# Performance work log

Hardware: AMD Instinct MI355X
Metric: run time of the kernel (lower is better)

Reference implementation:

```python
import jax, jax.numpy as jnp
import numpy as np

B, S, H = 2, 2048, 4096
NH, HD = 32, 128          # heads, head_dim = H // NH
ROPE_THETA = 10000.0
CLIP_QKV = 8.0
SCALE = HD ** -0.5


def setup_inputs() -> dict:
    key = jax.random.key(0)
    k1, k2, k3 = jax.random.split(key, 3)
    hidden_states = jax.random.normal(k1, (B, S, H), dtype=jnp.float32)
    positions = jnp.arange(S, dtype=jnp.int32)
    # 0.02 init scale keeps qkv magnitudes realistic so the +/-8 clamp rarely saturates
    w_qkv = jax.random.normal(k2, (3 * H, H), dtype=jnp.float32) * 0.02
    w_o = jax.random.normal(k3, (H, H), dtype=jnp.float32) * 0.02
    return {"hidden_states": hidden_states, "positions": positions,
            "w_qkv": w_qkv, "w_o": w_o}


def _rope(x, positions):
    # x: [B, S, NH, HD]; neox-style rotary over full head_dim
    half = HD // 2
    inv_freq = 1.0 / (ROPE_THETA ** (jnp.arange(0, half, dtype=jnp.float32) / half))
    ang = positions.astype(jnp.float32)[:, None] * inv_freq[None, :]  # [S, half]
    cos = jnp.cos(ang)[None, :, None, :]
    sin = jnp.sin(ang)[None, :, None, :]
    x1, x2 = x[..., :half], x[..., half:]
    return jnp.concatenate([x1 * cos - x2 * sin, x2 * cos + x1 * sin], axis=-1)


def reference(hidden_states, positions, w_qkv, w_o):
    # fused QKV projection (no bias) + clamp
    qkv = jnp.einsum('bsh,oh->bso', hidden_states, w_qkv)
    qkv = jnp.clip(qkv, -CLIP_QKV, CLIP_QKV)
    q, k, v = jnp.split(qkv, 3, axis=-1)            # each [B, S, H]
    q = q.reshape(B, S, NH, HD)
    k = k.reshape(B, S, NH, HD)
    v = v.reshape(B, S, NH, HD)
    q = _rope(q, positions)
    k = _rope(k, positions)
    # causal attention
    scores = jnp.einsum('bqhd,bkhd->bhqk', q, k) * SCALE
    causal = jnp.tril(jnp.ones((S, S), dtype=bool))
    scores = jnp.where(causal[None, None], scores, jnp.finfo(scores.dtype).min)
    probs = jax.nn.softmax(scores, axis=-1)
    attn = jnp.einsum('bhqk,bkhd->bqhd', probs, v).reshape(B, S, H)
    return jnp.einsum('bsh,oh->bso', attn, w_o)
```

## Files before the change

kernel.cpp:

```cpp
#include <hip/hip_runtime.h>
#include <hip/hip_bf16.h>

#define BATCH 2
#define SEQ 2048
#define HID 4096
#define NHEAD 32
#define HDIM 128
#define BH (BATCH*NHEAD)
#define MROWS (BATCH*SEQ)
#define ATT_SCALE 0.08838834764831845f

typedef __attribute__((ext_vector_type(8))) short bf16x8;
typedef __attribute__((ext_vector_type(4))) float f32x4;

__device__ __forceinline__ float bf2f(short x){
  union { float f; unsigned u; } v; v.u = ((unsigned)(unsigned short)x) << 16; return v.f;
}
__device__ __forceinline__ short f2bf(float f){
  union { float f; unsigned u; } v; v.f = f;
  unsigned r = v.u + 0x7fffu + ((v.u >> 16) & 1u);
  return (short)(r >> 16);
}
__device__ __forceinline__ void gload_lds16(const void* g, void* l){
  __builtin_amdgcn_global_load_lds(
    (const __attribute__((address_space(1))) void*)g,
    (__attribute__((address_space(3))) void*)l, 16, 0, 0);
}

__global__ void cvt_bf16(const float* __restrict__ in, short* __restrict__ out, int n4){
  int i = blockIdx.x*blockDim.x + threadIdx.x;
  int stride = gridDim.x*blockDim.x;
  for (; i < n4; i += stride){
    float4 v = ((const float4*)in)[i];
    short4 o;
    o.x = f2bf(v.x); o.y = f2bf(v.y); o.z = f2bf(v.z); o.w = f2bf(v.w);
    ((short4*)out)[i] = o;
  }
}

__global__ void rope_table_k(const int* __restrict__ pos, float* __restrict__ tab){
  int idx = blockIdx.x*blockDim.x + threadIdx.x;
  if (idx >= SEQ*64) return;
  int s = idx >> 6, d = idx & 63;
  float p = (float)pos[s];
  float inv = exp2f(-(float)d * (13.287712379549449f/64.0f));
  float ang = p * inv;
  tab[2*idx]   = cosf(ang);
  tab[2*idx+1] = sinf(ang);
}


template<int W>
__device__ __forceinline__ void stage_half(const short* __restrict__ gsrc, int ldg,
                                           short* lds, int tid, int h){
  #pragma unroll
  for (int li=0; li<2; ++li){
    int e16 = li*512 + tid;
    int rs = e16 >> 3, ck = e16 & 7;
    int r = ((rs/W)*2 + h)*W + (rs%W);
    gload_lds16(gsrc + (size_t)r*ldg + ((ck ^ (r&7))<<3),
                lds + r*64 + ck*8);
  }
}

__device__ __forceinline__ void read_ahalf(const short* Asb, int wr, int c, int g,
                                           int Mh, bf16x8 (&afr)[4][2]){
  #pragma unroll
  for (int mi=0; mi<4; ++mi){
    int row = wr*128 + (Mh*4+mi)*16 + c;
    const char* bp = (const char*)Asb + row*128;
    #pragma unroll
    for (int kk=0; kk<2; ++kk)
      afr[mi][kk] = *(const bf16x8*)(bp + ((kk*64 + g*16) ^ ((row&7)<<4)));
  }
}
__device__ __forceinline__ void read_bhalf(const short* Bsb, int wc, int c, int g,
                                           int Nh, bf16x8 (&bfr)[2][2]){
  #pragma unroll
  for (int ni=0; ni<2; ++ni){
    int row = wc*64 + (Nh*2+ni)*16 + c;
    const char* bp = (const char*)Bsb + row*128;
    #pragma unroll
    for (int kk=0; kk<2; ++kk)
      bfr[ni][kk] = *(const bf16x8*)(bp + ((kk*64 + g*16) ^ ((row&7)<<4)));
  }
}
template<int MH, int NHH>
__device__ __forceinline__ void mma_q(bf16x8 (&afr)[4][2], bf16x8 (&bfr)[2][2],
                                      f32x4 (&acc)[8][4]){
  #pragma unroll
  for (int kk=0; kk<2; ++kk)
    #pragma unroll
    for (int mi=0; mi<4; ++mi)
      #pragma unroll
      for (int ni=0; ni<2; ++ni)
        acc[MH*4+mi][NHH*2+ni] = __builtin_amdgcn_mfma_f32_16x16x32_bf16(
            afr[mi][kk], bfr[ni][kk], acc[MH*4+mi][NHH*2+ni], 0,0,0);
}

#define BAR()  asm volatile("s_barrier" ::: "memory")
#define LGK0() asm volatile("s_waitcnt lgkmcnt(0)" ::: "memory")
#define VMC6() asm volatile("s_waitcnt vmcnt(6)" ::: "memory")
#define VMC8() asm volatile("s_waitcnt vmcnt(8)" ::: "memory")
#define VMC0() asm volatile("s_waitcnt vmcnt(0)" ::: "memory")
#define SP1()  __builtin_amdgcn_s_setprio(1)
#define SP0()  __builtin_amdgcn_s_setprio(0)

template<int MODE>
__global__ __launch_bounds__(512, 2) void gemm8r(
    const short* __restrict__ A, const short* __restrict__ Bw,
    short* __restrict__ Qb, short* __restrict__ Kb, short* __restrict__ Vb,
    float* __restrict__ Of){
  __shared__ __align__(16) short As[2][256*64];
  __shared__ __align__(16) short Bs[2][256*64];
  const int K = HID;
  int tid = threadIdx.x, lane = tid & 63, w = tid >> 6;
  int wr = w >> 2, wc = w & 3, g = lane >> 4, c = lane & 15;
  int gx = gridDim.x;
  int nwg = gx * gridDim.y;
  int bid = blockIdx.y*gx + blockIdx.x;
  int cpx = nwg >> 3;
  int swz = (bid & 7)*cpx + (bid >> 3);
  int m0 = (swz / gx) * 256, n0 = (swz % gx) * 256;

  const short* Abase = A  + (size_t)m0*K;
  const short* Bbase = Bw + (size_t)n0*K;
  auto stageA = [&](int buf, int kt, int h){
    stage_half<64>(Abase + kt*64, K, &As[buf][0], tid, h);
  };
  auto stageB = [&](int buf, int kt, int h){
    stage_half<32>(Bbase + kt*64, K, &Bs[buf][0], tid, h);
  };

  f32x4 acc[8][4];
  f32x4 zero = {0.f,0.f,0.f,0.f};
  #pragma unroll
  for (int i=0;i<8;++i)
    #pragma unroll
    for (int j=0;j<4;++j) acc[i][j] = zero;
  bf16x8 afr[4][2], bfr0[2][2], bfr1[2][2];

  stageB(0,0,0); stageB(0,0,1); stageA(0,0,0); stageA(0,0,1);
  stageB(1,1,0); stageB(1,1,1); stageA(1,1,0); stageA(1,1,1);
  VMC8();
  BAR();

  const int NITER = K/128;
  for (int i = 0; i < NITER-1; ++i){
    int t2 = 2*i+2, t3 = 2*i+3;
    read_ahalf(&As[0][0], wr,c,g, 0, afr);
    read_bhalf(&Bs[0][0], wc,c,g, 0, bfr0);
    BAR(); LGK0(); SP1(); mma_q<0,0>(afr,bfr0,acc); SP0(); BAR();
    read_bhalf(&Bs[0][0], wc,c,g, 1, bfr1);
    stageB(0, t2, 0);
    BAR(); LGK0(); SP1(); mma_q<0,1>(afr,bfr1,acc); SP0(); BAR();
    read_ahalf(&As[0][0], wr,c,g, 1, afr);
    stageB(0, t2, 1); stageA(0, t2, 0);
    BAR(); LGK0(); SP1(); mma_q<1,1>(afr,bfr1,acc); SP0(); BAR();
    BAR(); LGK0(); SP1(); mma_q<1,0>(afr,bfr0,acc); SP0(); VMC6(); BAR();
    read_ahalf(&As[1][0], wr,c,g, 0, afr);
    read_bhalf(&Bs[1][0], wc,c,g, 0, bfr0);
    stageA(0, t2, 1);
    BAR(); LGK0(); SP1(); mma_q<0,0>(afr,bfr0,acc); SP0(); BAR();
    read_bhalf(&Bs[1][0], wc,c,g, 1, bfr1);
    stageB(1, t3, 0);
    BAR(); LGK0(); SP1(); mma_q<0,1>(afr,bfr1,acc); SP0(); BAR();
    read_ahalf(&As[1][0], wr,c,g, 1, afr);
    stageB(1, t3, 1); stageA(1, t3, 0);
    BAR(); LGK0(); SP1(); mma_q<1,1>(afr,bfr1,acc); SP0(); BAR();
    stageA(1, t3, 1);
    BAR(); LGK0(); SP1(); mma_q<1,0>(afr,bfr0,acc); SP0(); VMC8(); BAR();
  }
  {
    read_ahalf(&As[0][0], wr,c,g, 0, afr);
    read_bhalf(&Bs[0][0], wc,c,g, 0, bfr0);
    BAR(); LGK0(); SP1(); mma_q<0,0>(afr,bfr0,acc); SP0(); BAR();
    read_bhalf(&Bs[0][0], wc,c,g, 1, bfr1);
    BAR(); LGK0(); SP1(); mma_q<0,1>(afr,bfr1,acc); SP0(); BAR();
    read_ahalf(&As[0][0], wr,c,g, 1, afr);
    BAR(); LGK0(); SP1(); mma_q<1,1>(afr,bfr1,acc); SP0(); BAR();
    BAR(); LGK0(); SP1(); mma_q<1,0>(afr,bfr0,acc); SP0(); VMC0(); BAR();
    read_ahalf(&As[1][0], wr,c,g, 0, afr);
    read_bhalf(&Bs[1][0], wc,c,g, 0, bfr0);
    BAR(); LGK0(); SP1(); mma_q<0,0>(afr,bfr0,acc); SP0(); BAR();
    read_bhalf(&Bs[1][0], wc,c,g, 1, bfr1);
    BAR(); LGK0(); SP1(); mma_q<0,1>(afr,bfr1,acc); SP0(); BAR();
    read_ahalf(&As[1][0], wr,c,g, 1, afr);
    BAR(); LGK0(); SP1(); mma_q<1,1>(afr,bfr1,acc); SP0(); BAR();
    BAR(); LGK0(); SP1(); mma_q<1,0>(afr,bfr0,acc); SP0(); BAR();
  }

  #pragma unroll
  for (int fa=0; fa<8; ++fa){
    #pragma unroll
    for (int fb=0; fb<4; ++fb){
      f32x4 v = acc[fa][fb];
      #pragma unroll
      for (int rr=0; rr<4; ++rr){
        int row = m0 + wr*128 + fa*16 + g*4 + rr;
        int col = n0 + wc*64  + fb*16 + c;
        float x = v[rr];
        if (MODE == 0){
          x = fminf(fmaxf(x, -8.0f), 8.0f);
          int sel = col >> 12, wi = col & 4095;
          int head = wi >> 7, d = wi & 127;
          int b = row >> 11, s = row & 2047;
          size_t off = ((size_t)(b*NHEAD + head)*SEQ + s)*HDIM + d;
          short* dst = (sel == 0) ? Qb : (sel == 1) ? Kb : Vb;
          dst[off] = f2bf(x);
        } else {
          Of[(size_t)row*HID + col] = x;
        }
      }
    }
  }
}

__global__ void rope_apply_k(short* __restrict__ Qb, short* __restrict__ Kb,
                             const float* __restrict__ tab){
  int idx = blockIdx.x*blockDim.x + threadIdx.x;
  if (idx >= BH*SEQ*64) return;
  int d = idx & 63;
  int s = (idx >> 6) & (SEQ-1);
  int bh = idx >> 17;
  size_t base = ((size_t)bh*SEQ + s)*HDIM;
  float cs = tab[2*(s*64+d)], sn = tab[2*(s*64+d)+1];
  float q1 = bf2f(Qb[base+d]), q2 = bf2f(Qb[base+d+64]);
  Qb[base+d]    = f2bf(q1*cs - q2*sn);
  Qb[base+d+64] = f2bf(q2*cs + q1*sn);
  float k1 = bf2f(Kb[base+d]), k2 = bf2f(Kb[base+d+64]);
  Kb[base+d]    = f2bf(k1*cs - k2*sn);
  Kb[base+d+64] = f2bf(k2*cs + k1*sn);
}

__global__ void transpose_v_k(const short* __restrict__ V, short* __restrict__ Vt){
  __shared__ short t[32][33];
  int bh = blockIdx.z;
  int s0 = blockIdx.x*32, d0 = blockIdx.y*32;
  int tx = threadIdx.x & 31, ty = threadIdx.x >> 5;
  const short* src = V + ((size_t)bh*SEQ + s0)*HDIM + d0;
  #pragma unroll
  for (int i=ty;i<32;i+=8) t[i][tx] = src[(size_t)i*HDIM + tx];
  __syncthreads();
  short* dst = Vt + ((size_t)bh*HDIM + d0)*SEQ + s0;
  #pragma unroll
  for (int i=ty;i<32;i+=8) dst[(size_t)i*SEQ + tx] = t[tx][i];
}

__global__ __launch_bounds__(256) void flash_attn_k(
    const short* __restrict__ Qb, const short* __restrict__ Kb,
    const short* __restrict__ Vt, short* __restrict__ attn){
  __shared__ short Ks[2][64*128];
  __shared__ short Vs[2][128*64];
  __shared__ short Ps[4][16][72];
  int tid = threadIdx.x, lane = tid & 63, w = tid >> 6;
  int g = lane >> 4, c = lane & 15;
  int flat = blockIdx.y*gridDim.x + blockIdx.x;
  int xcd = flat & 7, idx = flat >> 3;
  int bh = xcd + 8*(idx >> 5);
  int qblk = idx & 31;
  int q0 = qblk * 64;
  int qw = q0 + w*16;
  bf16x8 qf[4];
  #pragma unroll
  for (int ks=0;ks<4;++ks)
    qf[ks] = *(const bf16x8*)(Qb + ((size_t)bh*SEQ + qw + c)*HDIM + ks*32 + g*8);
  f32x4 o[8];
  f32x4 zero = {0.f,0.f,0.f,0.f};
  #pragma unroll
  for (int i=0;i<8;++i) o[i] = zero;
  float m_r[4] = {-1e30f,-1e30f,-1e30f,-1e30f};
  float l_r[4] = {0.f,0.f,0.f,0.f};

  auto stage = [&](int j, int b){
    int kv0 = j*64;
    #pragma unroll
    for (int i=0;i<4;++i){
      int e = i*256 + tid;
      int kr = e >> 4, kc = e & 15;
      gload_lds16(Kb + ((size_t)bh*SEQ + kv0 + kr)*HDIM + (size_t)((kc ^ (kr&7))*8),
                  &Ks[b][kr*128 + kc*8]);
      int vr = e >> 3, vc = e & 7;
      gload_lds16(Vt + ((size_t)bh*HDIM + vr)*SEQ + kv0 + (size_t)((vc ^ (vr&7))*8),
                  &Vs[b][vr*64 + vc*8]);
    }
  };

  stage(0, 0);
  __syncthreads();
  int buf = 0;
  for (int j=0;j<=qblk;++j){
    if (j < qblk) stage(j+1, buf^1);

    int kv0 = j*64;
    f32x4 sf[4];
    #pragma unroll
    for (int fj=0;fj<4;++fj) sf[fj] = zero;
    __builtin_amdgcn_s_setprio(1);
    #pragma unroll
    for (int ks=0;ks<4;++ks){
      #pragma unroll
      for (int fj=0;fj<4;++fj){
        int kvrow = fj*16 + c;
        bf16x8 kb = *(const bf16x8*)&Ks[buf][kvrow*128 + (((ks*4+g) ^ (c&7))*8)];
        sf[fj] = __builtin_amdgcn_mfma_f32_16x16x32_bf16(qf[ks], kb, sf[fj], 0,0,0);
      }
    }
    __builtin_amdgcn_s_setprio(0);
    bool diag = (j == qblk);
    float rmax[4];
    #pragma unroll
    for (int rr=0;rr<4;++rr){
      #pragma unroll
      for (int fj=0;fj<4;++fj){
        float v = sf[fj][rr] * ATT_SCALE;
        if (diag && (kv0 + fj*16 + c) > (qw + g*4 + rr)) v = -1e30f;
        sf[fj][rr] = v;
      }
      float t = fmaxf(fmaxf(sf[0][rr], sf[1][rr]), fmaxf(sf[2][rr], sf[3][rr]));
      t = fmaxf(t, __shfl_xor(t, 1));
      t = fmaxf(t, __shfl_xor(t, 2));
      t = fmaxf(t, __shfl_xor(t, 4));
      t = fmaxf(t, __shfl_xor(t, 8));
      rmax[rr] = t;
    }
    float alpha[4];
    #pragma unroll
    for (int rr=0;rr<4;++rr){
      float mnew = fmaxf(m_r[rr], rmax[rr]);
      alpha[rr] = __expf(m_r[rr] - mnew);
      m_r[rr] = mnew;
      float ps = 0.f;
      #pragma unroll
      for (int fj=0;fj<4;++fj){
        float p = __expf(sf[fj][rr] - mnew);
        sf[fj][rr] = p;
        ps += p;
      }
      ps += __shfl_xor(ps, 1);
      ps += __shfl_xor(ps, 2);
      ps += __shfl_xor(ps, 4);
      ps += __shfl_xor(ps, 8);
      l_r[rr] = l_r[rr]*alpha[rr] + ps;
    }
    #pragma unroll
    for (int ni=0;ni<8;++ni){
      f32x4 t = o[ni];
      t[0]*=alpha[0]; t[1]*=alpha[1]; t[2]*=alpha[2]; t[3]*=alpha[3];
      o[ni] = t;
    }
    #pragma unroll
    for (int fj=0;fj<4;++fj)
      #pragma unroll
      for (int rr=0;rr<4;++rr)
        Ps[w][g*4+rr][fj*16+c] = f2bf(sf[fj][rr]);
    __builtin_amdgcn_s_setprio(1);
    #pragma unroll
    for (int ks=0;ks<2;++ks){
      bf16x8 pa = *(const bf16x8*)&Ps[w][c][ks*32 + g*8];
      #pragma unroll
      for (int ni=0;ni<8;++ni){
        int d = ni*16 + c;
        bf16x8 vb = *(const bf16x8*)&Vs[buf][d*64 + (((ks*4+g) ^ (c&7))*8)];
        o[ni] = __builtin_amdgcn_mfma_f32_16x16x32_bf16(pa, vb, o[ni], 0,0,0);
      }
    }
    __builtin_amdgcn_s_setprio(0);
    __syncthreads();
    buf ^= 1;
  }
  int b = bh >> 5, h = bh & 31;
  #pragma unroll
  for (int rr=0;rr<4;++rr){
    float inv = 1.0f / l_r[rr];
    int s = qw + g*4 + rr;
    #pragma unroll
    for (int ni=0;ni<8;++ni){
      int d = ni*16 + c;
      attn[((size_t)(b*SEQ + s))*HID + h*HDIM + d] = f2bf(o[ni][rr] * inv);
    }
  }
}

extern "C" void kernel_launch(void* const* d_in, const int* in_sizes, int n_in,
                              void* d_out, int out_size, void* d_ws, size_t ws_size,
                              hipStream_t stream){
  const float* hs   = (const float*)d_in[0];
  const int*   pos  = (const int*)d_in[1];
  const float* wqkv = (const float*)d_in[2];
  const float* wo   = (const float*)d_in[3];
  float* out = (float*)d_out;
  char* ws = (char*)d_ws;
  size_t off = 0;
  auto alloc = [&](size_t bytes){ void* p = ws + off; off += (bytes + 255) & ~(size_t)255; return p; };
  short* hsb   = (short*)alloc((size_t)MROWS*HID*2);
  short* wqkvb = (short*)alloc((size_t)3*HID*HID*2);
  short* wob   = (short*)alloc((size_t)HID*HID*2);
  short* Qb    = (short*)alloc((size_t)BH*SEQ*HDIM*2);
  short* Kb    = (short*)alloc((size_t)BH*SEQ*HDIM*2);
  short* Vb    = (short*)alloc((size_t)BH*SEQ*HDIM*2);
  short* Vt    = (short*)alloc((size_t)BH*SEQ*HDIM*2);
  short* attn  = (short*)alloc((size_t)MROWS*HID*2);
  float* tab   = (float*)alloc((size_t)SEQ*64*2*4);
  (void)ws_size; (void)in_sizes; (void)n_in; (void)out_size;

  cvt_bf16<<<1024,256,0,stream>>>(hs,   hsb,   MROWS*HID/4);
  cvt_bf16<<<2048,256,0,stream>>>(wqkv, wqkvb, 3*HID*HID/4);
  cvt_bf16<<<1024,256,0,stream>>>(wo,   wob,   HID*HID/4);
  rope_table_k<<<(SEQ*64+255)/256,256,0,stream>>>(pos, tab);
  gemm8r<0><<<dim3(48,16),512,0,stream>>>(hsb, wqkvb, Qb, Kb, Vb, nullptr);
  rope_apply_k<<<(BH*SEQ*64+255)/256,256,0,stream>>>(Qb, Kb, tab);
  transpose_v_k<<<dim3(SEQ/32, HDIM/32, BH),256,0,stream>>>(Vb, Vt);
  flash_attn_k<<<dim3(SEQ/64, BH),256,0,stream>>>(Qb, Kb, Vt, attn);
  gemm8r<1><<<dim3(16,16),512,0,stream>>>(attn, wob, nullptr, nullptr, nullptr, out);
}
```

Measured before the change: 817.5 us.

## Widen flash attention blocks, use exp2 with lazy rescale, vectorize rope, merge casts

Flash attention now runs 512-thread blocks covering 128 query rows, so each staged K/V tile serves twice as many queries. Per-warp early exit past the causal diagonal skips unneeded tiles. Softmax now uses exp2 with a log2e-folded scale and rescales the running max only when it grows by more than 8. The P buffer is XOR-swizzled instead of padded. Rope apply is vectorized to 8 elements per thread, and the three fp32-to-bf16 conversions become one launch; the lazy rescale relies on fp32 headroom and may change rounding slightly.

```diff
diff --git a/kernel.cpp b/kernel.cpp
--- a/kernel.cpp
+++ b/kernel.cpp
@@ -8,7 +8,7 @@
 #define HDIM 128
 #define BH (BATCH*NHEAD)
 #define MROWS (BATCH*SEQ)
-#define ATT_SCALE 0.08838834764831845f
+#define SC2 0.1275187963f
 
 typedef __attribute__((ext_vector_type(8))) short bf16x8;
 typedef __attribute__((ext_vector_type(4))) float f32x4;
@@ -27,14 +27,21 @@
     (__attribute__((address_space(3))) void*)l, 16, 0, 0);
 }
 
-__global__ void cvt_bf16(const float* __restrict__ in, short* __restrict__ out, int n4){
+__global__ void cvt3_bf16(const float* __restrict__ a, short* __restrict__ ao, int na4,
+                          const float* __restrict__ b, short* __restrict__ bo, int nb4,
+                          const float* __restrict__ cc, short* __restrict__ co, int nc4){
   int i = blockIdx.x*blockDim.x + threadIdx.x;
   int stride = gridDim.x*blockDim.x;
-  for (; i < n4; i += stride){
-    float4 v = ((const float4*)in)[i];
+  int tot = na4 + nb4 + nc4;
+  for (; i < tot; i += stride){
+    const float* src; short* dst; int k = i;
+    if (k < na4){ src=a; dst=ao; }
+    else if (k < na4+nb4){ k -= na4; src=b; dst=bo; }
+    else { k -= na4+nb4; src=cc; dst=co; }
+    float4 v = ((const float4*)src)[k];
     short4 o;
     o.x = f2bf(v.x); o.y = f2bf(v.y); o.z = f2bf(v.z); o.w = f2bf(v.w);
-    ((short4*)out)[i] = o;
+    ((short4*)dst)[k] = o;
   }
 }
 
@@ -48,7 +55,6 @@
   tab[2*idx]   = cosf(ang);
   tab[2*idx+1] = sinf(ang);
 }
-
 
 template<int W>
 __device__ __forceinline__ void stage_half(const short* __restrict__ gsrc, int ldg,
@@ -219,18 +225,25 @@
 __global__ void rope_apply_k(short* __restrict__ Qb, short* __restrict__ Kb,
                              const float* __restrict__ tab){
   int idx = blockIdx.x*blockDim.x + threadIdx.x;
-  if (idx >= BH*SEQ*64) return;
-  int d = idx & 63;
-  int s = (idx >> 6) & (SEQ-1);
-  int bh = idx >> 17;
-  size_t base = ((size_t)bh*SEQ + s)*HDIM;
-  float cs = tab[2*(s*64+d)], sn = tab[2*(s*64+d)+1];
-  float q1 = bf2f(Qb[base+d]), q2 = bf2f(Qb[base+d+64]);
-  Qb[base+d]    = f2bf(q1*cs - q2*sn);
-  Qb[base+d+64] = f2bf(q2*cs + q1*sn);
-  float k1 = bf2f(Kb[base+d]), k2 = bf2f(Kb[base+d+64]);
-  Kb[base+d]    = f2bf(k1*cs - k2*sn);
-  Kb[base+d+64] = f2bf(k2*cs + k1*sn);
+  if (idx >= BH*SEQ*8) return;
+  int t = idx & 7;
+  int s = (idx >> 3) & (SEQ-1);
+  int bh = idx >> 14;
+  size_t base = ((size_t)bh*SEQ + s)*HDIM + t*8;
+  const float* tb = tab + 2*(s*64 + t*8);
+  bf16x8 q1 = *(bf16x8*)(Qb+base), q2 = *(bf16x8*)(Qb+base+64);
+  bf16x8 k1 = *(bf16x8*)(Kb+base), k2 = *(bf16x8*)(Kb+base+64);
+  bf16x8 o1, o2, p1, p2;
+  #pragma unroll
+  for (int u=0;u<8;++u){
+    float cs = tb[2*u], sn = tb[2*u+1];
+    float a = bf2f(q1[u]), b = bf2f(q2[u]);
+    o1[u] = f2bf(a*cs - b*sn); o2[u] = f2bf(b*cs + a*sn);
+    a = bf2f(k1[u]); b = bf2f(k2[u]);
+    p1[u] = f2bf(a*cs - b*sn); p2[u] = f2bf(b*cs + a*sn);
+  }
+  *(bf16x8*)(Qb+base)    = o1; *(bf16x8*)(Qb+base+64) = o2;
+  *(bf16x8*)(Kb+base)    = p1; *(bf16x8*)(Kb+base+64) = p2;
 }
 
 __global__ void transpose_v_k(const short* __restrict__ V, short* __restrict__ Vt){
@@ -247,20 +260,19 @@
   for (int i=ty;i<32;i+=8) dst[(size_t)i*SEQ + tx] = t[tx][i];
 }
 
-__global__ __launch_bounds__(256) void flash_attn_k(
+__global__ __launch_bounds__(512, 4) void flash_attn2_k(
     const short* __restrict__ Qb, const short* __restrict__ Kb,
     const short* __restrict__ Vt, short* __restrict__ attn){
   __shared__ short Ks[2][64*128];
   __shared__ short Vs[2][128*64];
-  __shared__ short Ps[4][16][72];
+  __shared__ short Ps[8][16][64];
   int tid = threadIdx.x, lane = tid & 63, w = tid >> 6;
   int g = lane >> 4, c = lane & 15;
-  int flat = blockIdx.y*gridDim.x + blockIdx.x;
+  int flat = blockIdx.x;
   int xcd = flat & 7, idx = flat >> 3;
-  int bh = xcd + 8*(idx >> 5);
-  int qblk = idx & 31;
-  int q0 = qblk * 64;
-  int qw = q0 + w*16;
+  int bh = xcd + 8*(idx >> 4);
+  int jq = idx & 15;
+  int qw = jq*128 + w*16;
   bf16x8 qf[4];
   #pragma unroll
   for (int ks=0;ks<4;++ks)
@@ -275,8 +287,8 @@
   auto stage = [&](int j, int b){
     int kv0 = j*64;
     #pragma unroll
-    for (int i=0;i<4;++i){
-      int e = i*256 + tid;
+    for (int i=0;i<2;++i){
+      int e = i*512 + tid;
       int kr = e >> 4, kc = e & 15;
       gload_lds16(Kb + ((size_t)bh*SEQ + kv0 + kr)*HDIM + (size_t)((kc ^ (kr&7))*8),
                   &Ks[b][kr*128 + kc*8]);
@@ -286,86 +298,100 @@
     }
   };
 
+  const int jmaxb = 2*jq + 1;
+  const int jmaxw = (qw + 15) >> 6;
+
   stage(0, 0);
   __syncthreads();
   int buf = 0;
-  for (int j=0;j<=qblk;++j){
-    if (j < qblk) stage(j+1, buf^1);
-
-    int kv0 = j*64;
-    f32x4 sf[4];
-    #pragma unroll
-    for (int fj=0;fj<4;++fj) sf[fj] = zero;
-    __builtin_amdgcn_s_setprio(1);
-    #pragma unroll
-    for (int ks=0;ks<4;++ks){
-      #pragma unroll
-      for (int fj=0;fj<4;++fj){
-        int kvrow = fj*16 + c;
-        bf16x8 kb = *(const bf16x8*)&Ks[buf][kvrow*128 + (((ks*4+g) ^ (c&7))*8)];
-        sf[fj] = __builtin_amdgcn_mfma_f32_16x16x32_bf16(qf[ks], kb, sf[fj], 0,0,0);
-      }
+  for (int j=0; j<=jmaxb; ++j){
+    if (j < jmaxb) stage(j+1, buf^1);
+    if (j <= jmaxw){
+      int kv0 = j*64;
+      f32x4 sf[4];
+      #pragma unroll
+      for (int fj=0;fj<4;++fj) sf[fj] = zero;
+      __builtin_amdgcn_s_setprio(1);
+      #pragma unroll
+      for (int ks=0;ks<4;++ks){
+        #pragma unroll
+        for (int fj=0;fj<4;++fj){
+          int kvrow = fj*16 + c;
+          bf16x8 kb = *(const bf16x8*)&Ks[buf][kvrow*128 + (((ks*4+g) ^ (c&7))*8)];
+          sf[fj] = __builtin_amdgcn_mfma_f32_16x16x32_bf16(qf[ks], kb, sf[fj], 0,0,0);
+        }
+      }
+      __builtin_amdgcn_s_setprio(0);
+      bool diag = (j == jmaxw);
+      float rmax[4];
+      #pragma unroll
+      for (int rr=0;rr<4;++rr){
+        #pragma unroll
+        for (int fj=0;fj<4;++fj){
+          float v = sf[fj][rr] * SC2;
+          if (diag && (kv0 + fj*16 + c) > (qw + g*4 + rr)) v = -1e30f;
+          sf[fj][rr] = v;
+        }
+        float t = fmaxf(fmaxf(sf[0][rr], sf[1][rr]), fmaxf(sf[2][rr], sf[3][rr]));
+        t = fmaxf(t, __shfl_xor(t, 1));
+        t = fmaxf(t, __shfl_xor(t, 2));
+        t = fmaxf(t, __shfl_xor(t, 4));
+        t = fmaxf(t, __shfl_xor(t, 8));
+        rmax[rr] = t;
+      }
+      bool need = (rmax[0] > m_r[0] + 8.0f) | (rmax[1] > m_r[1] + 8.0f) |
+                  (rmax[2] > m_r[2] + 8.0f) | (rmax[3] > m_r[3] + 8.0f);
+      if (__any(need)){
+        float alpha[4];
+        #pragma unroll
+        for (int rr=0;rr<4;++rr){
+          float mnew = fmaxf(m_r[rr], rmax[rr]);
+          alpha[rr] = exp2f(m_r[rr] - mnew);
+          m_r[rr] = mnew;
+          l_r[rr] *= alpha[rr];
+        }
+        #pragma unroll
+        for (int ni=0;ni<8;++ni){
+          f32x4 t = o[ni];
+          t[0]*=alpha[0]; t[1]*=alpha[1]; t[2]*=alpha[2]; t[3]*=alpha[3];
+          o[ni] = t;
+        }
+      }
+      #pragma unroll
+      for (int rr=0;rr<4;++rr){
+        float ps = 0.f;
+        #pragma unroll
+        for (int fj=0;fj<4;++fj){
+          float p = exp2f(sf[fj][rr] - m_r[rr]);
+          sf[fj][rr] = p;
+          ps += p;
+        }
+        ps += __shfl_xor(ps, 1);
+        ps += __shfl_xor(ps, 2);
+        ps += __shfl_xor(ps, 4);
+        ps += __shfl_xor(ps, 8);
+        l_r[rr] += ps;
+      }
+      #pragma unroll
+      for (int fj=0;fj<4;++fj)
+        #pragma unroll
+        for (int rr=0;rr<4;++rr){
+          int row = g*4 + rr;
+          Ps[w][row][(fj*16+c) ^ ((row&7)<<3)] = f2bf(sf[fj][rr]);
+        }
+      __builtin_amdgcn_s_setprio(1);
+      #pragma unroll
+      for (int ks=0;ks<2;++ks){
+        bf16x8 pa = *(const bf16x8*)&Ps[w][c][(ks*32 + g*8) ^ ((c&7)<<3)];
+        #pragma unroll
+        for (int ni=0;ni<8;++ni){
+          int d = ni*16 + c;
+          bf16x8 vb = *(const bf16x8*)&Vs[buf][d*64 + (((ks*4+g) ^ (c&7))*8)];
+          o[ni] = __builtin_amdgcn_mfma_f32_16x16x32_bf16(pa, vb, o[ni], 0,0,0);
+        }
+      }
+      __builtin_amdgcn_s_setprio(0);
     }
-    __builtin_amdgcn_s_setprio(0);
-    bool diag = (j == qblk);
-    float rmax[4];
-    #pragma unroll
-    for (int rr=0;rr<4;++rr){
-      #pragma unroll
-      for (int fj=0;fj<4;++fj){
-        float v = sf[fj][rr] * ATT_SCALE;
-        if (diag && (kv0 + fj*16 + c) > (qw + g*4 + rr)) v = -1e30f;
-        sf[fj][rr] = v;
-      }
-      float t = fmaxf(fmaxf(sf[0][rr], sf[1][rr]), fmaxf(sf[2][rr], sf[3][rr]));
-      t = fmaxf(t, __shfl_xor(t, 1));
-      t = fmaxf(t, __shfl_xor(t, 2));
-      t = fmaxf(t, __shfl_xor(t, 4));
-      t = fmaxf(t, __shfl_xor(t, 8));
-      rmax[rr] = t;
-    }
-    float alpha[4];
-    #pragma unroll
-    for (int rr=0;rr<4;++rr){
-      float mnew = fmaxf(m_r[rr], rmax[rr]);
-      alpha[rr] = __expf(m_r[rr] - mnew);
-      m_r[rr] = mnew;
-      float ps = 0.f;
-      #pragma unroll
-      for (int fj=0;fj<4;++fj){
-        float p = __expf(sf[fj][rr] - mnew);
-        sf[fj][rr] = p;
-        ps += p;
-      }
-      ps += __shfl_xor(ps, 1);
-      ps += __shfl_xor(ps, 2);
-      ps += __shfl_xor(ps, 4);
-      ps += __shfl_xor(ps, 8);
-      l_r[rr] = l_r[rr]*alpha[rr] + ps;
-    }
-    #pragma unroll
-    for (int ni=0;ni<8;++ni){
-      f32x4 t = o[ni];
-      t[0]*=alpha[0]; t[1]*=alpha[1]; t[2]*=alpha[2]; t[3]*=alpha[3];
-      o[ni] = t;
-    }
-    #pragma unroll
-    for (int fj=0;fj<4;++fj)
-      #pragma unroll
-      for (int rr=0;rr<4;++rr)
-        Ps[w][g*4+rr][fj*16+c] = f2bf(sf[fj][rr]);
-    __builtin_amdgcn_s_setprio(1);
-    #pragma unroll
-    for (int ks=0;ks<2;++ks){
-      bf16x8 pa = *(const bf16x8*)&Ps[w][c][ks*32 + g*8];
-      #pragma unroll
-      for (int ni=0;ni<8;++ni){
-        int d = ni*16 + c;
-        bf16x8 vb = *(const bf16x8*)&Vs[buf][d*64 + (((ks*4+g) ^ (c&7))*8)];
-        o[ni] = __builtin_amdgcn_mfma_f32_16x16x32_bf16(pa, vb, o[ni], 0,0,0);
-      }
-    }
-    __builtin_amdgcn_s_setprio(0);
     __syncthreads();
     buf ^= 1;
   }
@@ -404,13 +430,13 @@
   float* tab   = (float*)alloc((size_t)SEQ*64*2*4);
   (void)ws_size; (void)in_sizes; (void)n_in; (void)out_size;
 
-  cvt_bf16<<<1024,256,0,stream>>>(hs,   hsb,   MROWS*HID/4);
-  cvt_bf16<<<2048,256,0,stream>>>(wqkv, wqkvb, 3*HID*HID/4);
-  cvt_bf16<<<1024,256,0,stream>>>(wo,   wob,   HID*HID/4);
+  cvt3_bf16<<<2048,256,0,stream>>>(hs, hsb, MROWS*HID/4,
+                                   wqkv, wqkvb, 3*HID*HID/4,
+                                   wo, wob, HID*HID/4);
   rope_table_k<<<(SEQ*64+255)/256,256,0,stream>>>(pos, tab);
   gemm8r<0><<<dim3(48,16),512,0,stream>>>(hsb, wqkvb, Qb, Kb, Vb, nullptr);
-  rope_apply_k<<<(BH*SEQ*64+255)/256,256,0,stream>>>(Qb, Kb, tab);
+  rope_apply_k<<<(BH*SEQ*8+255)/256,256,0,stream>>>(Qb, Kb, tab);
   transpose_v_k<<<dim3(SEQ/32, HDIM/32, BH),256,0,stream>>>(Vb, Vt);
-  flash_attn_k<<<dim3(SEQ/64, BH),256,0,stream>>>(Qb, Kb, Vt, attn);
+  flash_attn2_k<<<dim3(BH*16),512,0,stream>>>(Qb, Kb, Vt, attn);
   gemm8r<1><<<dim3(16,16),512,0,stream>>>(attn, wob, nullptr, nullptr, nullptr, out);
 }
```

New measurement: 830.6 us. No clear change (+1.6%).
